# Optimization experiments

Hardware: AMD Instinct MI355X
Metric: run time of the kernel (lower is better)

Reference implementation:

```python
import jax, jax.numpy as jnp
import numpy as np

K = 256      # embedding size k
STATE = 128  # latent state size
IN = 64      # external input size
OBS = 64     # observation size
L = 512      # sequence length (time-major)
B = 256      # batch size


def _glorot(key, shape):
    return jax.random.normal(key, shape, dtype=jnp.float32) / float(np.sqrt(shape[0]))


def setup_inputs():
    key = jax.random.key(0)
    ks = jax.random.split(key, 12)
    p = {}
    p["external_input_seq"] = jax.random.normal(ks[0], (L, B, IN), dtype=jnp.float32)
    p["observations_seq"] = jax.random.normal(ks[1], (L, B, OBS), dtype=jnp.float32)
    p["eps"] = jax.random.normal(ks[2], (L, B, STATE), dtype=jnp.float32)  # reparam noise
    # PreProcess: Linear + tanh
    p["Wu"] = _glorot(ks[3], (IN, K)); p["bu"] = jnp.zeros((K,), jnp.float32)
    p["Wx"] = _glorot(ks[4], (OBS, K)); p["bx"] = jnp.zeros((K,), jnp.float32)
    # input_rnn: vanilla tanh RNN, 1 layer, k -> k
    p["W_ih"] = _glorot(ks[5], (K, K)); p["b_ih"] = jnp.zeros((K,), jnp.float32)
    p["W_hh"] = _glorot(ks[6], (K, K)); p["b_hh"] = jnp.zeros((K,), jnp.float32)
    # posterior_a_layer: MLP(2k, k, k, 1) = Linear -> tanh -> Linear
    p["Wa1"] = _glorot(ks[7], (2 * K, K)); p["ba1"] = jnp.zeros((K,), jnp.float32)
    p["Wa2"] = _glorot(ks[8], (K, K)); p["ba2"] = jnp.zeros((K,), jnp.float32)

    def dblock_params(k1, in_dim, hid, out):
        kk = jax.random.split(k1, 4)
        return (_glorot(kk[0], (in_dim, hid)), jnp.zeros((hid,), jnp.float32),
                _glorot(kk[1], (in_dim, hid)), jnp.zeros((hid,), jnp.float32),
                _glorot(kk[2], (hid, out)), jnp.zeros((out,), jnp.float32),
                _glorot(kk[3], (hid, out)), jnp.zeros((out,), jnp.float32))

    names = ["f1_W", "f1_b", "f2_W", "f2_b", "mu_W", "mu_b", "ls_W", "ls_b"]
    for pref, kk in (("post_", ks[9]), ("prior_", ks[10])):
        vals = dblock_params(kk, STATE + K, 2 * K, STATE)
        for n, v in zip(names, vals):
            p[pref + n] = v
    return p


def _dblock(x, f1_W, f1_b, f2_W, f2_b, mu_W, mu_b, ls_W, ls_b):
    # TD-VAE DBlock: gated hidden, then mu / logsigma heads
    t = jnp.tanh(x @ f1_W + f1_b) * jax.nn.sigmoid(x @ f2_W + f2_b)
    return t @ mu_W + mu_b, t @ ls_W + ls_b


def reference(external_input_seq, observations_seq, eps, Wu, bu, Wx, bx,
              W_ih, b_ih, W_hh, b_hh, Wa1, ba1, Wa2, ba2,
              post_f1_W, post_f1_b, post_f2_W, post_f2_b, post_mu_W, post_mu_b, post_ls_W, post_ls_b,
              prior_f1_W, prior_f1_b, prior_f2_W, prior_f2_b, prior_mu_W, prior_mu_b, prior_ls_W, prior_ls_b):
    batch = external_input_seq.shape[1]
    u_emb = jnp.tanh(external_input_seq @ Wu + bu)   # [L,B,K]
    x_emb = jnp.tanh(observations_seq @ Wx + bx)     # [L,B,K]

    # input_rnn (tanh RNN) over time, d0 = 0 (memory_state=None)
    def rnn_step(d, x):
        d_new = jnp.tanh(x @ W_ih + b_ih + d @ W_hh + b_hh)
        return d_new, d_new
    d0 = jnp.zeros((batch, W_hh.shape[0]), dtype=u_emb.dtype)
    dn, d_seq = jax.lax.scan(rnn_step, d0, u_emb)    # dn [B,K], d_seq [L,B,K]

    # posterior_a_layer: pointwise MLP; flip(0) then flip(0) is a no-op for a pointwise map
    ad = jnp.concatenate([d_seq, x_emb], axis=-1)    # [L,B,2K]
    a_seq = jnp.tanh(ad @ Wa1 + ba1) @ Wa2 + ba2     # [L,B,K]

    state_size = post_mu_W.shape[1]
    z0 = jnp.zeros((batch, state_size), dtype=u_emb.dtype)

    def step(z_prev, inp):
        a_t, d_t, e_t = inp
        mean_res, logsigma = _dblock(jnp.concatenate([z_prev, a_t], axis=-1),
                                     post_f1_W, post_f1_b, post_f2_W, post_f2_b,
                                     post_mu_W, post_mu_b, post_ls_W, post_ls_b)
        prior_mean = _dblock(jnp.concatenate([z_prev, d_t], axis=-1),
                             prior_f1_W, prior_f1_b, prior_f2_W, prior_f2_b,
                             prior_mu_W, prior_mu_b, prior_ls_W, prior_ls_b)[0]
        mu = prior_mean + mean_res
        # cov = diag(exp(logsigma)) -> std = exp(0.5*logsigma); reparameterized sample
        z_new = mu + jnp.exp(0.5 * logsigma) * e_t
        return z_new, (mu, logsigma)

    zn, (state_mu, state_logsigma) = jax.lax.scan(step, z0, (a_seq, d_seq, eps))
    return state_mu, state_logsigma, dn, zn
```

## Files before the change

### kernel.cpp

```cpp
#include <hip/hip_runtime.h>

#define LSEQ 512
#define BATCH 256
#define KDIM 256
#define STATE 128

using f32x4  = __attribute__((ext_vector_type(4))) float;
using short8 = __attribute__((ext_vector_type(8))) short;
using u32x2  = __attribute__((ext_vector_type(2))) unsigned int;
using u32x4  = __attribute__((ext_vector_type(4))) unsigned int;

__device__ __forceinline__ float bf2f(unsigned short u){
  return __uint_as_float(((unsigned int)u) << 16);
}
__device__ __forceinline__ unsigned short f2bf(float f){
  unsigned int u = __float_as_uint(f);
  u += 0x7FFFu + ((u >> 16) & 1u);
  return (unsigned short)(u >> 16);
}
__device__ __forceinline__ float fast_tanh(float x){
  float ax = fabsf(x);
  float e  = __expf(2.0f * ax);
  float t  = 1.0f - 2.0f / (e + 1.0f);
  return copysignf(t, x);
}
__device__ __forceinline__ float fast_sig(float x){
  return 1.0f / (1.0f + __expf(-x));
}
__device__ __forceinline__ f32x4 mfma16(short8 a, short8 b, f32x4 c){
  return __builtin_amdgcn_mfma_f32_16x16x32_bf16(a, b, c, 0, 0, 0);
}

__device__ __forceinline__ int swz128 (int b){ return b ^ ((((b >> 7) & 7) << 4)); }
__device__ __forceinline__ int swz256 (int b){ return b ^ ((((b >> 8) & 7) << 4)); }
__device__ __forceinline__ int swz512 (int b){ return b ^ ((((b >> 9) & 7) << 4)); }

__device__ __forceinline__ void st_b128_ic(void* p, u32x4 v){
  asm volatile("global_store_dwordx4 %0, %1, off sc0 sc1" :: "v"(p), "v"(v) : "memory");
}
__device__ __forceinline__ void st_b64_ic(void* p, u32x2 v){
  asm volatile("global_store_dwordx2 %0, %1, off sc0 sc1" :: "v"(p), "v"(v) : "memory");
}
#define LD2_IC(dst, p) asm volatile("global_load_dwordx2 %0, %1, off sc0 sc1" : "=v"(dst) : "v"(p) : "memory")

__device__ __forceinline__ f32x4 cvt4(u32x2 q){
  f32x4 r;
  r[0] = __uint_as_float(q[0] << 16);
  r[1] = __uint_as_float(q[0] & 0xFFFF0000u);
  r[2] = __uint_as_float(q[1] << 16);
  r[3] = __uint_as_float(q[1] & 0xFFFF0000u);
  return r;
}

struct WDesc { const float* src; unsigned short* dst; int K, N, ld, rowoff, coloff; };
struct WDescs { WDesc d[24]; };

__global__ __launch_bounds__(256,4) void convert_weights(WDescs ds){
  WDesc w = ds.d[blockIdx.y];
  int total = w.K * w.N;
  int idx = blockIdx.x * 256 + threadIdx.x;
  if (idx < total){
    int n = idx / w.K;
    int k = idx - n * w.K;
    w.dst[idx] = f2bf(w.src[(size_t)(w.rowoff + k) * w.ld + w.coloff + n]);
  }
}

__global__ __launch_bounds__(256,1) void init_flags(int* flags){
  flags[blockIdx.x * 256 + threadIdx.x] = 0;
}

struct GArg {
  const void* A; const unsigned short* Bt; const float* bias; const float* bias2;
  unsigned short* C; int lda, ldc, coff, K, act, a_f32;
};
struct GArgs { GArg g[4]; };

__global__ __launch_bounds__(256,2) void gemm_multi(GArgs args){
  GArg ga = args.g[blockIdx.z];
  __shared__ __align__(16) unsigned short lsA[128*64];
  __shared__ __align__(16) unsigned short lsB[128*64];
  const int tid  = threadIdx.x;
  const int wave = tid >> 6, lane = tid & 63;
  const int col_l = lane & 15, rgrp = lane >> 4;
  const int m0 = blockIdx.x * 128, n0 = blockIdx.y * 128;
  const int wm = (wave >> 1) * 64, wn = (wave & 1) * 64;

  f32x4 acc[4][4];
  const f32x4 z4 = {0.f,0.f,0.f,0.f};
  #pragma unroll
  for (int i=0;i<4;i++){ acc[i][0]=z4; acc[i][1]=z4; acc[i][2]=z4; acc[i][3]=z4; }

  const int srow = tid >> 1;
  const int sbe  = (tid & 1) * 32;

  for (int k0 = 0; k0 < ga.K; k0 += 64){
    uint4 av[4], bv[4];
    if (ga.a_f32){
      const float* Ap = (const float*)ga.A + (size_t)(m0 + srow) * ga.lda + k0 + sbe;
      uint4 fv[8];
      #pragma unroll
      for (int i=0;i<8;i++) fv[i] = *(const uint4*)((const char*)Ap + i*16);
      #pragma unroll
      for (int i=0;i<4;i++){
        const float* f = (const float*)&fv[i*2];
        uint4 o;
        o.x = (unsigned)f2bf(f[0]) | ((unsigned)f2bf(f[1]) << 16);
        o.y = (unsigned)f2bf(f[2]) | ((unsigned)f2bf(f[3]) << 16);
        o.z = (unsigned)f2bf(f[4]) | ((unsigned)f2bf(f[5]) << 16);
        o.w = (unsigned)f2bf(f[6]) | ((unsigned)f2bf(f[7]) << 16);
        av[i] = o;
      }
    } else {
      const unsigned short* Ap = (const unsigned short*)ga.A + (size_t)(m0 + srow) * ga.lda + k0 + sbe;
      #pragma unroll
      for (int i=0;i<4;i++) av[i] = *(const uint4*)((const char*)Ap + i*16);
    }
    const unsigned short* Bp = ga.Bt + (size_t)(n0 + srow) * ga.K + k0 + sbe;
    #pragma unroll
    for (int i=0;i<4;i++) bv[i] = *(const uint4*)((const char*)Bp + i*16);

    __syncthreads();
    #pragma unroll
    for (int i=0;i<4;i++){
      *(uint4*)((char*)lsA + swz128(srow*128 + sbe*2 + i*16)) = av[i];
      *(uint4*)((char*)lsB + swz128(srow*128 + sbe*2 + i*16)) = bv[i];
    }
    __syncthreads();
    #pragma unroll
    for (int kk=0; kk<2; kk++){
      short8 af[4], bfr[4];
      #pragma unroll
      for (int mt=0; mt<4; mt++)
        af[mt] = *(const short8*)((const char*)lsA + swz128((wm + mt*16 + col_l)*128 + kk*64 + rgrp*16));
      #pragma unroll
      for (int nt=0; nt<4; nt++)
        bfr[nt] = *(const short8*)((const char*)lsB + swz128((wn + nt*16 + col_l)*128 + kk*64 + rgrp*16));
      #pragma unroll
      for (int mt=0; mt<4; mt++)
        #pragma unroll
        for (int nt=0; nt<4; nt++)
          acc[mt][nt] = mfma16(af[mt], bfr[nt], acc[mt][nt]);
    }
  }
  #pragma unroll
  for (int nt=0; nt<4; nt++){
    int col = n0 + wn + nt*16 + col_l;
    const float* bsrc = (col < 512) ? ga.bias : ga.bias2;
    float bb = bsrc ? bsrc[col & 511] : 0.0f;
    #pragma unroll
    for (int mt=0; mt<4; mt++){
      #pragma unroll
      for (int r=0; r<4; r++){
        int row = m0 + wm + mt*16 + rgrp*4 + r;
        float v = acc[mt][nt][r] + bb;
        if (ga.act == 1) v = fast_tanh(v);
        ga.C[(size_t)row * ga.ldc + ga.coff + col] = f2bf(v);
      }
    }
  }
}

struct GArg2 {
  const unsigned short* A; const unsigned short* Bt; const float* bias; const float* bias2;
  unsigned short* C; int lda, ldc, coff, K, act;
};
struct GArgs2 { GArg2 g[2]; };

__global__ __launch_bounds__(256,2) void gemm_glds(GArgs2 args){
  GArg2 ga = args.g[blockIdx.z];
  __shared__ __align__(16) unsigned short ls[4][128*64];
  const int tid  = threadIdx.x;
  const int wave = tid >> 6, lane = tid & 63;
  const int col_l = lane & 15, rgrp = lane >> 4;
  const int m0 = blockIdx.x * 128, n0 = blockIdx.y * 128;
  const int wm = (wave >> 1) * 64, wn = (wave & 1) * 64;

  const int lrow = lane >> 3;
  const int scol = (((lane & 7) ^ lrow) << 3);

  auto STAGE = [&](int k0, int buf){
    #pragma unroll
    for (int c = 0; c < 4; c++){
      int srow = wave*32 + c*8 + lrow;
      const unsigned short* pa = ga.A  + (size_t)(m0 + srow) * ga.lda + k0 + scol;
      const unsigned short* pb = ga.Bt + (size_t)(n0 + srow) * ga.K  + k0 + scol;
      __builtin_amdgcn_global_load_lds(
          (const __attribute__((address_space(1))) unsigned int*)pa,
          (__attribute__((address_space(3))) unsigned int*)((char*)&ls[buf*2][0]   + wave*4096 + c*1024),
          16, 0, 0);
      __builtin_amdgcn_global_load_lds(
          (const __attribute__((address_space(1))) unsigned int*)pb,
          (__attribute__((address_space(3))) unsigned int*)((char*)&ls[buf*2+1][0] + wave*4096 + c*1024),
          16, 0, 0);
    }
  };

  f32x4 acc[4][4];
  const f32x4 z4 = {0.f,0.f,0.f,0.f};
  #pragma unroll
  for (int i=0;i<4;i++){ acc[i][0]=z4; acc[i][1]=z4; acc[i][2]=z4; acc[i][3]=z4; }

  const int niter = ga.K >> 6;
  STAGE(0, 0);

  for (int i = 0; i < niter; i++){
    if (i + 1 < niter){
      STAGE((i+1)*64, (i+1) & 1);
      asm volatile("s_waitcnt vmcnt(8)" ::: "memory");
    } else {
      asm volatile("s_waitcnt vmcnt(0)" ::: "memory");
    }
    __syncthreads();
    const char* la = (const char*)&ls[(i&1)*2][0];
    const char* lb = (const char*)&ls[(i&1)*2+1][0];
    #pragma unroll
    for (int kk=0; kk<2; kk++){
      short8 af[4], bfr[4];
      #pragma unroll
      for (int mt=0; mt<4; mt++)
        af[mt] = *(const short8*)(la + swz128((wm + mt*16 + col_l)*128 + kk*64 + rgrp*16));
      #pragma unroll
      for (int nt=0; nt<4; nt++)
        bfr[nt] = *(const short8*)(lb + swz128((wn + nt*16 + col_l)*128 + kk*64 + rgrp*16));
      #pragma unroll
      for (int mt=0; mt<4; mt++)
        #pragma unroll
        for (int nt=0; nt<4; nt++)
          acc[mt][nt] = mfma16(af[mt], bfr[nt], acc[mt][nt]);
    }
    __syncthreads();
  }

  #pragma unroll
  for (int nt=0; nt<4; nt++){
    int col = n0 + wn + nt*16 + col_l;
    const float* bsrc = (col < 512) ? ga.bias : ga.bias2;
    float bb = bsrc ? bsrc[col & 511] : 0.0f;
    #pragma unroll
    for (int mt=0; mt<4; mt++){
      #pragma unroll
      for (int r=0; r<4; r++){
        int row = m0 + wm + mt*16 + rgrp*4 + r;
        float v = acc[mt][nt][r] + bb;
        if (ga.act == 1) v = fast_tanh(v);
        ga.C[(size_t)row * ga.ldc + ga.coff + col] = f2bf(v);
      }
    }
  }
}

__global__ __launch_bounds__(256,1) void rnn_chunk(
    const unsigned short* __restrict__ rnn_in,
    const unsigned short* __restrict__ Whh_t,
    const float* __restrict__ b_hh,
    unsigned short* __restrict__ cat_d,
    float* __restrict__ dn_out,
    unsigned short* __restrict__ d_state,
    int t0, int nsteps)
{
  __shared__ __align__(16) unsigned short dls[16*256];
  const int tid = threadIdx.x, wave = tid >> 6, lane = tid & 63;
  const int col_l = lane & 15, rgrp = lane >> 4;
  const int brow0 = blockIdx.x * 16;
  const int ncol = wave * 64;

  short8 bfr[4][8];
  #pragma unroll
  for (int nt=0; nt<4; nt++){
    const unsigned short* bp = Whh_t + (size_t)(ncol + nt*16 + col_l) * 256;
    #pragma unroll
    for (int kk=0; kk<8; kk++)
      bfr[nt][kk] = *(const short8*)(bp + kk*32 + rgrp*8);
  }
  float bias[4];
  #pragma unroll
  for (int nt=0; nt<4; nt++) bias[nt] = b_hh[ncol + nt*16 + col_l];

  if (t0 == 0){
    for (int i = tid; i < 16*256; i += 256){
      int row = i >> 8, col = i & 255;
      *(unsigned short*)((char*)dls + swz512(row*512 + col*2)) = 0;
    }
  } else {
    const unsigned short* ds = d_state + (size_t)brow0 * 256;
    for (int i = tid; i < 16*256; i += 256){
      int row = i >> 8, col = i & 255;
      *(unsigned short*)((char*)dls + swz512(row*512 + col*2)) = ds[row*256 + col];
    }
  }
  __syncthreads();

  for (int tl=0; tl<nsteps; tl++){
    unsigned short rv[4][4];
    const unsigned short* rp = rnn_in + (size_t)(tl*BATCH + brow0) * 256;
    #pragma unroll
    for (int nt=0; nt<4; nt++)
      #pragma unroll
      for (int r=0; r<4; r++)
        rv[nt][r] = rp[(size_t)(rgrp*4 + r)*256 + ncol + nt*16 + col_l];

    f32x4 acc[4];
    const f32x4 z4 = {0.f,0.f,0.f,0.f};
    acc[0]=z4; acc[1]=z4; acc[2]=z4; acc[3]=z4;
    #pragma unroll
    for (int kk=0; kk<8; kk++){
      short8 af = *(const short8*)((const char*)dls + swz512((lane & 15)*512 + kk*64 + rgrp*16));
      #pragma unroll
      for (int nt=0; nt<4; nt++)
        acc[nt] = mfma16(af, bfr[nt][kk], acc[nt]);
    }
    __syncthreads();
    #pragma unroll
    for (int nt=0; nt<4; nt++){
      #pragma unroll
      for (int r=0; r<4; r++){
        float h = acc[nt][r] + bf2f(rv[nt][r]) + bias[nt];
        float d = fast_tanh(h);
        int row = rgrp*4 + r, col = ncol + nt*16 + col_l;
        unsigned short db = f2bf(d);
        *(unsigned short*)((char*)dls + swz512(row*512 + col*2)) = db;
        cat_d[(size_t)(tl*BATCH + brow0 + row)*512 + col] = db;
        if (t0 + tl == LSEQ-1) dn_out[(size_t)(brow0 + row)*256 + col] = d;
      }
    }
    __syncthreads();
  }
  unsigned short* dso = d_state + (size_t)brow0 * 256;
  for (int i = tid; i < 16*256; i += 256){
    int row = i >> 8, col = i & 255;
    dso[row*256 + col] = *(const unsigned short*)((const char*)dls + swz512(row*512 + col*2));
  }
}

__global__ __launch_bounds__(512,1) void zrec_mb(
    const unsigned short* __restrict__ preP, const unsigned short* __restrict__ preQ,
    const unsigned short* __restrict__ Wzz,
    const unsigned short* __restrict__ W2,
    const float* __restrict__ pmub, const float* __restrict__ plsb, const float* __restrict__ qmub,
    const float* __restrict__ eps,
    float* __restrict__ out_mu, float* __restrict__ out_ls, float* __restrict__ out_zn,
    unsigned short* __restrict__ z_state,
    unsigned short* __restrict__ mb, int* __restrict__ flags,
    int t0, int nsteps, int fbase)
{
  __shared__ __align__(16) unsigned short zls[16*128];
  __shared__ __align__(16) unsigned short tls[16*256];
  const int tid = threadIdx.x, wave = tid >> 6, lane = tid & 63;
  const int col_l = lane & 15, rgrp = lane >> 4;
  const int bid = blockIdx.x;
  const int c   = (bid >> 3) & 3;
  const int g   = (bid & 7) + ((bid >> 5) << 3);
  const int brow0 = g * 16;
  const int NT2 = (c < 2) ? 2 : 1;

  const unsigned short* pre = (c < 2) ? preP : preQ;
  const int cb = (c & 1) * 256;

  short8 w1[2][2][4];
  {
    const unsigned short* wz = Wzz + (size_t)c * 65536;
    #pragma unroll
    for (int m=0; m<2; m++)
      #pragma unroll
      for (int nt=0; nt<2; nt++){
        int n = wave*32 + nt*16 + col_l;
        #pragma unroll
        for (int kk=0; kk<4; kk++)
          w1[m][nt][kk] = *(const short8*)(wz + (size_t)(m*256 + n)*128 + kk*32 + rgrp*8);
      }
  }
  short8 w2r[2][8];
  {
    const unsigned short* wp = W2 + (size_t)c * 65536;
    #pragma unroll
    for (int nt=0; nt<2; nt++){
      if (nt < NT2){
        int ccol = wave*(16*((c<2)?2:1)) + nt*16;
        int mat = (c < 2) ? (ccol >> 7) : 0;
        int n   = (ccol & 127) + col_l;
        #pragma unroll
        for (int kk=0; kk<8; kk++)
          w2r[nt][kk] = *(const short8*)(wp + (size_t)(mat*128 + n)*256 + kk*32 + rgrp*8);
      }
    }
  }
  int* const myflag = flags + (g*4 + c)*32;

  if (t0 == 0){
    for (int i = tid; i < 16*128; i += 512){
      int row = i >> 7, col = i & 127;
      *(unsigned short*)((char*)zls + swz256(row*256 + col*2)) = 0;
    }
  } else {
    const unsigned short* zs = z_state + (size_t)brow0 * 128;
    for (int i = tid; i < 16*128; i += 512){
      int row = i >> 7, col = i & 127;
      *(unsigned short*)((char*)zls + swz256(row*256 + col*2)) = zs[row*128 + col];
    }
  }
  __syncthreads();

  auto LD_PRE = [&](int tl, unsigned short (&pa_)[2][4], unsigned short (&pb_)[2][4]){
    const unsigned short* bA = pre + ((size_t)tl*BATCH + brow0)*1024 + cb;
    #pragma unroll
    for (int nt=0; nt<2; nt++)
      #pragma unroll
      for (int r=0; r<4; r++){
        int row = rgrp*4 + r, col = wave*32 + nt*16 + col_l;
        pa_[nt][r] = bA[(size_t)row*1024 + col];
        pb_[nt][r] = bA[(size_t)row*1024 + 512 + col];
      }
  };

  const int rrow = tid >> 5;
  const int rc0  = (tid & 31) * 4;
  const f32x4 bp4 = *(const f32x4*)(pmub + rc0);
  const f32x4 bl4 = *(const f32x4*)(plsb + rc0);
  const f32x4 bq4 = *(const f32x4*)(qmub + rc0);

  unsigned short pa0[2][4], pb0[2][4], pa1[2][4], pb1[2][4];
  LD_PRE(0, pa0, pb0);

  const f32x4 z4 = {0.f,0.f,0.f,0.f};
  for (int tl=0; tl<nsteps; ++tl){
    size_t growr = (size_t)(t0+tl)*BATCH + brow0 + rrow;
    f32x4 er = *(const f32x4*)(eps + growr*STATE + rc0);
    int nx = (tl+1 < nsteps) ? tl+1 : tl;
    LD_PRE(nx, pa1, pb1);

    short8 af1[4];
    #pragma unroll
    for (int kk=0; kk<4; kk++)
      af1[kk] = *(const short8*)((const char*)zls + swz256((lane & 15)*256 + kk*64 + rgrp*16));
    f32x4 a1[2][2];
    a1[0][0]=z4; a1[0][1]=z4; a1[1][0]=z4; a1[1][1]=z4;
    #pragma unroll
    for (int kk=0; kk<4; kk++)
      #pragma unroll
      for (int m=0; m<2; m++)
        #pragma unroll
        for (int nt=0; nt<2; nt++)
          a1[m][nt] = mfma16(af1[kk], w1[m][nt][kk], a1[m][nt]);

    #pragma unroll
    for (int nt=0; nt<2; nt++)
      #pragma unroll
      for (int r=0; r<4; r++){
        float h1 = a1[0][nt][r] + bf2f(pa0[nt][r]);
        float h2 = a1[1][nt][r] + bf2f(pb0[nt][r]);
        float tv = fast_tanh(h1) * fast_sig(h2);
        int row = rgrp*4 + r, tcol = wave*32 + nt*16 + col_l;
        *(unsigned short*)((char*)tls + swz512(row*512 + tcol*2)) = f2bf(tv);
      }
    __syncthreads();

    f32x4 a2[2];
    a2[0]=z4; a2[1]=z4;
    #pragma unroll
    for (int kk=0; kk<8; kk++){
      short8 af2 = *(const short8*)((const char*)tls + swz512((lane & 15)*512 + kk*64 + rgrp*16));
      #pragma unroll
      for (int nt=0; nt<2; nt++)
        if (nt < NT2) a2[nt] = mfma16(af2, w2r[nt][kk], a2[nt]);
    }
    __syncthreads();

    if (c < 2){
      #pragma unroll
      for (int nt=0; nt<2; nt++)
        #pragma unroll
        for (int r=0; r<4; r++)
          tls[(rgrp*4 + r)*256 + wave*32 + nt*16 + col_l] = f2bf(a2[nt][r]);
    } else {
      #pragma unroll
      for (int r=0; r<4; r++)
        tls[(rgrp*4 + r)*128 + wave*16 + col_l] = f2bf(a2[0][r]);
    }
    __syncthreads();

    unsigned short* slot = mb + (size_t)((g*2 + (tl & 1))*4 + c)*4096;
    if (c < 2){
      u32x4 v = *(const u32x4*)((const char*)tls + tid*16);
      st_b128_ic(slot + tid*8, v);
    } else {
      u32x2 v = *(const u32x2*)((const char*)tls + tid*8);
      st_b64_ic(slot + tid*4, v);
    }
    asm volatile("s_waitcnt vmcnt(0)" ::: "memory");
    __syncthreads();
    const int target = fbase + tl + 1;
    if (tid == 0)
      __hip_atomic_store(myflag, target, __ATOMIC_RELAXED, __HIP_MEMORY_SCOPE_AGENT);

    if (wave == 7 && lane < 3){
      const int* pf = flags + (g*4 + ((c + 1 + lane) & 3))*32;
      while (__hip_atomic_load(pf, __ATOMIC_RELAXED, __HIP_MEMORY_SCOPE_AGENT) < target)
        __builtin_amdgcn_s_sleep(1);
    }
    __syncthreads();

    const unsigned short* mbb = mb + (size_t)((g*2 + (tl & 1))*4)*4096;
    const unsigned short* s0 = mbb;
    const unsigned short* s1 = mbb + 4096;
    const unsigned short* s2 = mbb + 8192;
    const unsigned short* s3 = mbb + 12288;
    u32x2 q0,q1,q2,q3,q4,q5;
    LD2_IC(q0, s0 + rrow*256 + rc0);
    LD2_IC(q1, s1 + rrow*256 + rc0);
    LD2_IC(q2, s0 + rrow*256 + 128 + rc0);
    LD2_IC(q3, s1 + rrow*256 + 128 + rc0);
    LD2_IC(q4, s2 + rrow*128 + rc0);
    LD2_IC(q5, s3 + rrow*128 + rc0);
    asm volatile("s_waitcnt vmcnt(0)" ::: "memory");
    __builtin_amdgcn_sched_barrier(0);

    f32x4 mup = cvt4(q0) + cvt4(q1);
    f32x4 lsv = cvt4(q2) + cvt4(q3) + bl4;
    f32x4 muq = cvt4(q4) + cvt4(q5);
    f32x4 muv = (muq + bq4) + (mup + bp4);
    f32x4 zv;
    #pragma unroll
    for (int i=0; i<4; i++) zv[i] = muv[i] + __expf(0.5f * lsv[i]) * er[i];

    unsigned int lo = (unsigned)f2bf(zv[0]) | ((unsigned)f2bf(zv[1]) << 16);
    unsigned int hi = (unsigned)f2bf(zv[2]) | ((unsigned)f2bf(zv[3]) << 16);
    uint2 zp; zp.x = lo; zp.y = hi;
    *(uint2*)((char*)zls + swz256(rrow*256 + rc0*2)) = zp;
    if (c == 0){
      *(f32x4*)(out_mu + growr*STATE + rc0) = muv;
      *(f32x4*)(out_ls + growr*STATE + rc0) = lsv;
      if (t0 + tl == LSEQ-1)
        *(f32x4*)(out_zn + ((size_t)(brow0 + rrow))*STATE + rc0) = zv;
    }
    __syncthreads();

    #pragma unroll
    for (int nt=0; nt<2; nt++)
      #pragma unroll
      for (int r=0; r<4; r++){ pa0[nt][r] = pa1[nt][r]; pb0[nt][r] = pb1[nt][r]; }
  }

  if (c == 0){
    unsigned short* zso = z_state + (size_t)brow0 * 128;
    for (int i = tid; i < 16*128; i += 512){
      int row = i >> 7, col = i & 127;
      zso[row*128 + col] = *(const unsigned short*)((const char*)zls + swz256(row*256 + col*2));
    }
  }
}

extern "C" void kernel_launch(void* const* d_in, const int* in_sizes, int n_in,
                              void* d_out, int out_size, void* d_ws, size_t ws_size,
                              hipStream_t stream)
{
  const float* ext = (const float*)d_in[0];
  const float* obs = (const float*)d_in[1];
  const float* eps = (const float*)d_in[2];
  const float* Wu  = (const float*)d_in[3];
  const float* bu  = (const float*)d_in[4];
  const float* Wx  = (const float*)d_in[5];
  const float* bx  = (const float*)d_in[6];
  const float* W_ih= (const float*)d_in[7];
  const float* b_ih= (const float*)d_in[8];
  const float* W_hh= (const float*)d_in[9];
  const float* b_hh= (const float*)d_in[10];
  const float* Wa1 = (const float*)d_in[11];
  const float* ba1 = (const float*)d_in[12];
  const float* Wa2 = (const float*)d_in[13];
  const float* ba2 = (const float*)d_in[14];
  const float* pf1W= (const float*)d_in[15]; const float* pf1b = (const float*)d_in[16];
  const float* pf2W= (const float*)d_in[17]; const float* pf2b = (const float*)d_in[18];
  const float* pmuW= (const float*)d_in[19]; const float* pmub = (const float*)d_in[20];
  const float* plsW= (const float*)d_in[21]; const float* plsb = (const float*)d_in[22];
  const float* qf1W= (const float*)d_in[23]; const float* qf1b = (const float*)d_in[24];
  const float* qf2W= (const float*)d_in[25]; const float* qf2b = (const float*)d_in[26];
  const float* qmuW= (const float*)d_in[27]; const float* qmub = (const float*)d_in[28];

  int NC = 0;
  const int cands[7] = {1,2,4,8,16,32,64};
  size_t rows = 0;
  for (int ci=0; ci<7; ci++){
    size_t r = (size_t)(LSEQ/cands[ci])*BATCH;
    size_t elems = 3400000 + r*3072;
    if (elems * 2 <= ws_size){ NC = cands[ci]; rows = r; break; }
  }
  if (!NC) return;
  const int nsteps = LSEQ/NC;
  const int gx = (int)(rows/128);

  unsigned short* ws = (unsigned short*)d_ws;
  size_t off = 0;
  auto alloc = [&](size_t elems){
    unsigned short* p = ws + off;
    off += (elems + 127) & ~(size_t)127;
    return p;
  };

  unsigned short* Wu_t  = alloc(64*256);
  unsigned short* Wx_t  = alloc(64*256);
  unsigned short* Wih_t = alloc(256*256);
  unsigned short* Whh_t = alloc(256*256);
  unsigned short* Wa1_t = alloc(512*256);
  unsigned short* Wa2_t = alloc(256*256);
  unsigned short* fAp   = alloc(1024*256);
  unsigned short* fAq   = alloc(1024*256);
  unsigned short* Wzz   = alloc(4*2*256*128);
  unsigned short* W2z   = alloc(4*2*128*256);
  unsigned short* d_state = alloc(256*256);
  unsigned short* z_state = alloc(256*128);
  unsigned short* mbx  = alloc(16*2*4*4096);
  int*   flg  = (int*)alloc(4096);
  unsigned short* bufA  = alloc(rows*256);
  unsigned short* bufB  = alloc(rows*256);
  unsigned short* bufC  = alloc(rows*512);
  unsigned short* preP  = alloc(rows*1024);
  unsigned short* preQ  = alloc(rows*1024);
  if (off * sizeof(unsigned short) > ws_size) return;

  float* out_mu = (float*)d_out;
  float* out_ls = out_mu + (size_t)LSEQ*BATCH*STATE;
  float* out_dn = out_ls + (size_t)LSEQ*BATCH*STATE;
  float* out_zn = out_dn + (size_t)BATCH*KDIM;

  WDescs wd;
  int wi = 0;
  auto add = [&](const float* s, unsigned short* d, int Kk, int Nn, int ld, int ro, int co){
    wd.d[wi].src = s; wd.d[wi].dst = d; wd.d[wi].K = Kk; wd.d[wi].N = Nn;
    wd.d[wi].ld = ld; wd.d[wi].rowoff = ro; wd.d[wi].coloff = co; wi++;
  };
  add(Wu,   Wu_t,  64, 256, 256, 0, 0);
  add(Wx,   Wx_t,  64, 256, 256, 0, 0);
  add(W_ih, Wih_t, 256, 256, 256, 0, 0);
  add(W_hh, Whh_t, 256, 256, 256, 0, 0);
  add(Wa1,  Wa1_t, 512, 256, 256, 0, 0);
  add(Wa2,  Wa2_t, 256, 256, 256, 0, 0);
  add(pf1W, fAp,            256, 512, 512, 128, 0);
  add(pf2W, fAp + 512*256,  256, 512, 512, 128, 0);
  add(qf1W, fAq,            256, 512, 512, 128, 0);
  add(qf2W, fAq + 512*256,  256, 512, 512, 128, 0);
  for (int c=0; c<4; c++){
    const float* s1 = (c < 2) ? pf1W : qf1W;
    const float* s2 = (c < 2) ? pf2W : qf2W;
    add(s1, Wzz + (size_t)(c*2+0)*32768, 128, 256, 512, 0, (c&1)*256);
    add(s2, Wzz + (size_t)(c*2+1)*32768, 128, 256, 512, 0, (c&1)*256);
  }
  add(pmuW, W2z + (size_t)(0*2+0)*32768, 256, 128, 128, 0,   0);
  add(plsW, W2z + (size_t)(0*2+1)*32768, 256, 128, 128, 0,   0);
  add(pmuW, W2z + (size_t)(1*2+0)*32768, 256, 128, 128, 256, 0);
  add(plsW, W2z + (size_t)(1*2+1)*32768, 256, 128, 128, 256, 0);
  add(qmuW, W2z + (size_t)(2*2+0)*32768, 256, 128, 128, 0,   0);
  add(qmuW, W2z + (size_t)(3*2+0)*32768, 256, 128, 128, 256, 0);

  convert_weights<<<dim3(512,24), 256, 0, stream>>>(wd);
  init_flags<<<8, 256, 0, stream>>>(flg);

  for (int c=0; c<NC; ++c){
    const int t0 = c * nsteps;
    const size_t row0 = (size_t)t0 * BATCH;

    GArgs e{};
    e.g[0] = GArg{ext + row0*64, Wu_t, bu, bu, bufA, 64, 256, 0,   64, 1, 1};
    e.g[1] = GArg{obs + row0*64, Wx_t, bx, bx, bufC, 64, 512, 256, 64, 1, 1};
    gemm_multi<<<dim3(gx,2,2), 256, 0, stream>>>(e);

    GArgs2 rn{};
    rn.g[0] = GArg2{bufA, Wih_t, b_ih, b_ih, bufB, 256, 256, 0, 256, 0};
    gemm_glds<<<dim3(gx,2,1), 256, 0, stream>>>(rn);

    rnn_chunk<<<16, 256, 0, stream>>>(bufB, Whh_t, b_hh, bufC, out_dn, d_state, t0, nsteps);

    GArgs2 a1{};
    a1.g[0] = GArg2{bufC, Wa1_t, ba1, ba1, bufA, 512, 256, 0, 512, 1};
    gemm_glds<<<dim3(gx,2,1), 256, 0, stream>>>(a1);

    GArgs2 a2{};
    a2.g[0] = GArg2{bufA, Wa2_t, ba2, ba2, bufB, 256, 256, 0, 256, 0};
    gemm_glds<<<dim3(gx,2,1), 256, 0, stream>>>(a2);

    GArgs2 pr{};
    pr.g[0] = GArg2{bufB, fAp, pf1b, pf2b, preP, 256, 1024, 0, 256, 0};
    pr.g[1] = GArg2{bufC, fAq, qf1b, qf2b, preQ, 512, 1024, 0, 256, 0};
    gemm_glds<<<dim3(gx,8,2), 256, 0, stream>>>(pr);

    zrec_mb<<<64, 512, 0, stream>>>(preP, preQ, Wzz, W2z,
                                    pmub, plsb, qmub, eps, out_mu, out_ls, out_zn,
                                    z_state, mbx, flg, t0, nsteps, c*nsteps);
  }
}
```

Baseline: 3.622 ms.

## Fold Wa2 into posterior f1/f2 weights and streamline recurrence flag sync

Precomputes a composed weight GA = Wa2·fAp and a matching bias so the a2 GEMM per chunk is removed, and the posterior pre-activation GEMM reads the tanh output directly. In the recurrent kernel, the second-layer results are written to a separate LDS buffer so one barrier can be dropped. The four per-group flags now share one cache line, so each wave polls all peers with a single dwordx4 load instead of one wave polling and then a block barrier. The trade-off is extra rounding from the bf16 composed weights and a per-wave spin on every step.

```diff
diff --git a/kernel.cpp b/kernel.cpp
--- a/kernel.cpp
+++ b/kernel.cpp
@@ -68,6 +68,27 @@
 
 __global__ __launch_bounds__(256,1) void init_flags(int* flags){
   flags[blockIdx.x * 256 + threadIdx.x] = 0;
+}
+
+__global__ __launch_bounds__(256,4) void compose_GA(
+    const float* __restrict__ Wa2, const float* __restrict__ ba2,
+    const unsigned short* __restrict__ fAp,
+    const float* __restrict__ pf1b, const float* __restrict__ pf2b,
+    unsigned short* __restrict__ GA,
+    float* __restrict__ gb)
+{
+  const int n = blockIdx.x;
+  const int k2 = threadIdx.x;
+  const unsigned short* fr = fAp + (size_t)n * 256;
+  const float* wr = Wa2 + (size_t)k2 * 256;
+  float s = 0.f;
+  for (int j = 0; j < 256; j++) s += wr[j] * bf2f(fr[j]);
+  GA[(size_t)n * 256 + k2] = f2bf(s);
+  if (k2 == 0){
+    float b = 0.f;
+    for (int j = 0; j < 256; j++) b += ba2[j] * bf2f(fr[j]);
+    gb[n] = b + ((n < 512) ? pf1b[n] : pf2b[n - 512]);
+  }
 }
 
 struct GArg {
@@ -346,6 +367,7 @@
 {
   __shared__ __align__(16) unsigned short zls[16*128];
   __shared__ __align__(16) unsigned short tls[16*256];
+  __shared__ __align__(16) unsigned short bls[16*256];
   const int tid = threadIdx.x, wave = tid >> 6, lane = tid & 63;
   const int col_l = lane & 15, rgrp = lane >> 4;
   const int bid = blockIdx.x;
@@ -385,7 +407,8 @@
       }
     }
   }
-  int* const myflag = flags + (g*4 + c)*32;
+  int* const fline  = flags + g*32;
+  int* const myflag = fline + c;
 
   if (t0 == 0){
     for (int i = tid; i < 16*128; i += 512){
@@ -464,27 +487,25 @@
       for (int nt=0; nt<2; nt++)
         if (nt < NT2) a2[nt] = mfma16(af2, w2r[nt][kk], a2[nt]);
     }
-    __syncthreads();
-
     if (c < 2){
       #pragma unroll
       for (int nt=0; nt<2; nt++)
         #pragma unroll
         for (int r=0; r<4; r++)
-          tls[(rgrp*4 + r)*256 + wave*32 + nt*16 + col_l] = f2bf(a2[nt][r]);
+          bls[(rgrp*4 + r)*256 + wave*32 + nt*16 + col_l] = f2bf(a2[nt][r]);
     } else {
       #pragma unroll
       for (int r=0; r<4; r++)
-        tls[(rgrp*4 + r)*128 + wave*16 + col_l] = f2bf(a2[0][r]);
+        bls[(rgrp*4 + r)*128 + wave*16 + col_l] = f2bf(a2[0][r]);
     }
     __syncthreads();
 
     unsigned short* slot = mb + (size_t)((g*2 + (tl & 1))*4 + c)*4096;
     if (c < 2){
-      u32x4 v = *(const u32x4*)((const char*)tls + tid*16);
+      u32x4 v = *(const u32x4*)((const char*)bls + tid*16);
       st_b128_ic(slot + tid*8, v);
     } else {
-      u32x2 v = *(const u32x2*)((const char*)tls + tid*8);
+      u32x2 v = *(const u32x2*)((const char*)bls + tid*8);
       st_b64_ic(slot + tid*4, v);
     }
     asm volatile("s_waitcnt vmcnt(0)" ::: "memory");
@@ -493,12 +514,19 @@
     if (tid == 0)
       __hip_atomic_store(myflag, target, __ATOMIC_RELAXED, __HIP_MEMORY_SCOPE_AGENT);
 
-    if (wave == 7 && lane < 3){
-      const int* pf = flags + (g*4 + ((c + 1 + lane) & 3))*32;
-      while (__hip_atomic_load(pf, __ATOMIC_RELAXED, __HIP_MEMORY_SCOPE_AGENT) < target)
+    if (lane == 0){
+      u32x4 F;
+      for (;;){
+        asm volatile("global_load_dwordx4 %0, %1, off sc0 sc1\n\ts_waitcnt vmcnt(0)"
+                     : "=v"(F) : "v"(fline) : "memory");
+        int ok = 1;
+        #pragma unroll
+        for (int p=0; p<4; p++)
+          if (p != c && (int)F[p] < target) ok = 0;
+        if (ok) break;
         __builtin_amdgcn_s_sleep(1);
-    }
-    __syncthreads();
+      }
+    }
 
     const unsigned short* mbb = mb + (size_t)((g*2 + (tl & 1))*4)*4096;
     const unsigned short* s0 = mbb;
@@ -605,6 +633,8 @@
   unsigned short* Wa2_t = alloc(256*256);
   unsigned short* fAp   = alloc(1024*256);
   unsigned short* fAq   = alloc(1024*256);
+  unsigned short* GAp   = alloc(1024*256);
+  float*          gbp   = (float*)alloc(2048);
   unsigned short* Wzz   = alloc(4*2*256*128);
   unsigned short* W2z   = alloc(4*2*128*256);
   unsigned short* d_state = alloc(256*256);
@@ -653,6 +683,7 @@
   add(qmuW, W2z + (size_t)(3*2+0)*32768, 256, 128, 128, 256, 0);
 
   convert_weights<<<dim3(512,24), 256, 0, stream>>>(wd);
+  compose_GA<<<1024, 256, 0, stream>>>(Wa2, ba2, fAp, pf1b, pf2b, GAp, gbp);
   init_flags<<<8, 256, 0, stream>>>(flg);
 
   for (int c=0; c<NC; ++c){
@@ -674,12 +705,8 @@
     a1.g[0] = GArg2{bufC, Wa1_t, ba1, ba1, bufA, 512, 256, 0, 512, 1};
     gemm_glds<<<dim3(gx,2,1), 256, 0, stream>>>(a1);
 
-    GArgs2 a2{};
-    a2.g[0] = GArg2{bufA, Wa2_t, ba2, ba2, bufB, 256, 256, 0, 256, 0};
-    gemm_glds<<<dim3(gx,2,1), 256, 0, stream>>>(a2);
-
     GArgs2 pr{};
-    pr.g[0] = GArg2{bufB, fAp, pf1b, pf2b, preP, 256, 1024, 0, 256, 0};
+    pr.g[0] = GArg2{bufA, GAp, gbp, gbp + 512, preP, 256, 1024, 0, 256, 0};
     pr.g[1] = GArg2{bufC, fAq, qf1b, qf2b, preQ, 512, 1024, 0, 256, 0};
     gemm_glds<<<dim3(gx,8,2), 256, 0, stream>>>(pr);
 
```

Result: no change. 3.630 ms (+0.2%).
